# Optimization experiments

Measured on AMD Instinct MI355X. Metric: run time of the kernel, lower is better.

Reference implementation:

```python
import jax, jax.numpy as jnp
import numpy as np

Y_SCALE = 0.01  # fixed weight quantization scale (q_scale of the int8 weights)


def setup_inputs() -> dict:
    key = jax.random.key(0)
    kx, kw, kb = jax.random.split(key, 3)
    B, S, IN, OUT = 4, 2048, 4096, 4096
    x = jax.random.normal(kx, (B, S, IN), dtype=jnp.float32)
    # int8 quantized weights, stored transposed as (in_features, out_features)
    weight_q = jax.random.randint(kw, (IN, OUT), -128, 128, dtype=jnp.int32)
    bias = jax.random.normal(kb, (OUT,), dtype=jnp.float32)
    return {"x": x, "weight_q": weight_q, "bias": bias}


def reference(x, weight_q, bias):
    # Per-batch-sample dynamic activation scale: max(|x_i|)/128 over each [S, IN] slice
    x_scale = jnp.max(jnp.abs(x), axis=(1, 2), keepdims=True) / 128.0  # [B,1,1]
    # int8 quantize: round + clip
    xq = jnp.clip(jnp.round(x / x_scale), -128, 127).astype(jnp.int8)  # [B,S,IN]
    wq = weight_q.astype(jnp.int8)                                      # [IN,OUT]
    c = jax.lax.dot_general(
        xq, wq,
        dimension_numbers=(((2,), (0,)), ((), ())),
        preferred_element_type=jnp.int32,
    )  # [B,S,OUT]
    # dequantize and bias-add
    y = c.astype(jnp.float32) * (x_scale * Y_SCALE)
    return y + bias
```

## Files before the change

kernel.cpp:

```cpp
#include <hip/hip_runtime.h>
#include <stdint.h>

#define K_DIM 4096
#define N_DIM 4096
#define M_DIM 8192
#define S_ROWS 2048
#define NBATCH 4

typedef int v4i __attribute__((ext_vector_type(4)));

__device__ __forceinline__ void gload16(const void* g, void* l) {
    __builtin_amdgcn_global_load_lds(
        (const __attribute__((address_space(1))) unsigned int*)g,
        (__attribute__((address_space(3))) unsigned int*)l, 16, 0, 0);
}

__global__ void absmax_kernel(const float* __restrict__ x, unsigned* __restrict__ amax) {
    int b = blockIdx.y;
    const float4* xb = (const float4*)(x + (size_t)b * S_ROWS * K_DIM);
    int tid = blockIdx.x * 256 + threadIdx.x;
    const int stride = 1024 * 256;
    float m = 0.f;
#pragma unroll
    for (int i = 0; i < 8; ++i) {
        float4 v = xb[tid + i * stride];
        m = fmaxf(m, fmaxf(fmaxf(fabsf(v.x), fabsf(v.y)),
                           fmaxf(fabsf(v.z), fabsf(v.w))));
    }
#pragma unroll
    for (int off = 32; off; off >>= 1)
        m = fmaxf(m, __shfl_xor(m, off));
    __shared__ float red[4];
    if ((threadIdx.x & 63) == 0) red[threadIdx.x >> 6] = m;
    __syncthreads();
    if (threadIdx.x == 0) {
        m = fmaxf(fmaxf(red[0], red[1]), fmaxf(red[2], red[3]));
        atomicMax(&amax[b], __float_as_uint(m));
    }
}

__global__ void quant_kernel(const float* __restrict__ x,
                             const unsigned* __restrict__ amax,
                             char* __restrict__ xq) {
    size_t gid = (size_t)blockIdx.x * 256 + threadIdx.x;
    size_t base = gid * 16;
    int b = (int)(base >> 23);
    float inv = 128.0f / __uint_as_float(amax[b]);
    const float4* xs = (const float4*)(x + base);
    unsigned parts[4];
#pragma unroll
    for (int i = 0; i < 4; ++i) {
        float4 v = xs[i];
        int q0 = max(-128, min(127, (int)rintf(v.x * inv)));
        int q1 = max(-128, min(127, (int)rintf(v.y * inv)));
        int q2 = max(-128, min(127, (int)rintf(v.z * inv)));
        int q3 = max(-128, min(127, (int)rintf(v.w * inv)));
        parts[i] = (q0 & 255) | ((q1 & 255) << 8) | ((q2 & 255) << 16) | ((q3 & 255) << 24);
    }
    *(uint4*)(xq + base) = make_uint4(parts[0], parts[1], parts[2], parts[3]);
}

__global__ void wtrans_kernel(const int* __restrict__ wq, char* __restrict__ wt) {
    __shared__ unsigned lds[64 * 17];
    int t = threadIdx.x;
    int c = t & 63;
    int g = t >> 6;
    int n0 = blockIdx.x * 64;
    int k0 = blockIdx.y * 64;
#pragma unroll
    for (int rep = 0; rep < 4; ++rep) {
        int kb = g * 16 + rep * 4;
        int v0 = wq[(size_t)(k0 + kb + 0) * N_DIM + n0 + c];
        int v1 = wq[(size_t)(k0 + kb + 1) * N_DIM + n0 + c];
        int v2 = wq[(size_t)(k0 + kb + 2) * N_DIM + n0 + c];
        int v3 = wq[(size_t)(k0 + kb + 3) * N_DIM + n0 + c];
        lds[c * 17 + (kb >> 2)] =
            (v0 & 255) | ((v1 & 255) << 8) | ((v2 & 255) << 16) | ((v3 & 255) << 24);
    }
    __syncthreads();
    int row = t >> 2;
    int ch = t & 3;
    uint4 o;
    o.x = lds[row * 17 + ch * 4 + 0];
    o.y = lds[row * 17 + ch * 4 + 1];
    o.z = lds[row * 17 + ch * 4 + 2];
    o.w = lds[row * 17 + ch * 4 + 3];
    *(uint4*)(wt + (size_t)(n0 + row) * K_DIM + k0 + ch * 16) = o;
}

__global__ void gemm_kernel(const char* __restrict__ A,
                            const char* __restrict__ Bt,
                            const float* __restrict__ bias,
                            const unsigned* __restrict__ amax,
                            float* __restrict__ out) {
    __shared__ char As[128 * 64];
    __shared__ char Bs[128 * 64];
    int t = threadIdx.x;
    int l = t & 63;
    int w = t >> 6;
    int wm = w >> 1, wn = w & 1;
    int m0 = blockIdx.y * 128;
    int n0 = blockIdx.x * 128;

    v4i acc[4][4];
#pragma unroll
    for (int i = 0; i < 4; ++i)
#pragma unroll
        for (int j = 0; j < 4; ++j)
            acc[i][j] = (v4i){0, 0, 0, 0};

    int sk = l >> 4;
    int rb = l & 15;

    for (int kt = 0; kt < K_DIM; kt += 64) {
#pragma unroll
        for (int i = 0; i < 2; ++i) {
            int p = (w * 2 + i) * 64 + l;
            int r = p >> 2;
            int s = (p & 3) ^ ((r >> 1) & 3);
            gload16(A + (size_t)(m0 + r) * K_DIM + kt + s * 16, As + p * 16);
            gload16(Bt + (size_t)(n0 + r) * K_DIM + kt + s * 16, Bs + p * 16);
        }
        __syncthreads();

        v4i a[4], bf[4];
#pragma unroll
        for (int mi = 0; mi < 4; ++mi) {
            int row = wm * 64 + mi * 16 + rb;
            a[mi] = *(const v4i*)(As + row * 64 + ((sk ^ ((row >> 1) & 3)) << 4));
        }
#pragma unroll
        for (int ni = 0; ni < 4; ++ni) {
            int row = wn * 64 + ni * 16 + rb;
            bf[ni] = *(const v4i*)(Bs + row * 64 + ((sk ^ ((row >> 1) & 3)) << 4));
        }
#pragma unroll
        for (int mi = 0; mi < 4; ++mi)
#pragma unroll
            for (int ni = 0; ni < 4; ++ni)
                acc[mi][ni] = __builtin_amdgcn_mfma_i32_16x16x64_i8(
                    a[mi], bf[ni], acc[mi][ni], 0, 0, 0);
        __syncthreads();
    }

    float scale = __uint_as_float(amax[m0 >> 11]) * (1.0f / 128.0f) * 0.01f;
    int colb = n0 + wn * 64 + (l & 15);
    int rowb = m0 + wm * 64 + (l >> 4) * 4;
#pragma unroll
    for (int ni = 0; ni < 4; ++ni) {
        float bv = bias[colb + ni * 16];
#pragma unroll
        for (int mi = 0; mi < 4; ++mi) {
#pragma unroll
            for (int rg = 0; rg < 4; ++rg) {
                out[(size_t)(rowb + mi * 16 + rg) * N_DIM + colb + ni * 16] =
                    (float)acc[mi][ni][rg] * scale + bv;
            }
        }
    }
}

extern "C" void kernel_launch(void* const* d_in, const int* in_sizes, int n_in,
                              void* d_out, int out_size, void* d_ws, size_t ws_size,
                              hipStream_t stream) {
    const float* x = (const float*)d_in[0];
    const int* wq = (const int*)d_in[1];
    const float* bias = (const float*)d_in[2];
    float* out = (float*)d_out;

    unsigned* amax = (unsigned*)d_ws;
    char* xq = (char*)d_ws + 256;
    char* wt = (char*)d_ws + 256 + (size_t)M_DIM * K_DIM;

    hipMemsetAsync(d_ws, 0, 16, stream);

    wtrans_kernel<<<dim3(64, 64), 256, 0, stream>>>(wq, wt);
    absmax_kernel<<<dim3(1024, 4), 256, 0, stream>>>(x, amax);
    quant_kernel<<<8192, 256, 0, stream>>>(x, amax, xq);
    gemm_kernel<<<dim3(32, 64), 256, 0, stream>>>(xq, wt, bias, amax, out);
}
```

Baseline: 264.9 us.

## Replace int8 GEMM with 256x256 double-buffered, phase-pipelined 8-wave kernel

```diff
diff --git a/kernel.cpp b/kernel.cpp
--- a/kernel.cpp
+++ b/kernel.cpp
@@ -5,7 +5,7 @@
 #define N_DIM 4096
 #define M_DIM 8192
 #define S_ROWS 2048
-#define NBATCH 4
+#define NT 32
 
 typedef int v4i __attribute__((ext_vector_type(4)));
 
@@ -13,6 +13,12 @@
     __builtin_amdgcn_global_load_lds(
         (const __attribute__((address_space(1))) unsigned int*)g,
         (__attribute__((address_space(3))) unsigned int*)l, 16, 0, 0);
+}
+
+__device__ __forceinline__ void barrier() {
+    asm volatile("" ::: "memory");
+    __builtin_amdgcn_s_barrier();
+    asm volatile("" ::: "memory");
 }
 
 __global__ void absmax_kernel(const float* __restrict__ x, unsigned* __restrict__ amax) {
@@ -88,76 +94,173 @@
     *(uint4*)(wt + (size_t)(n0 + row) * K_DIM + k0 + ch * 16) = o;
 }
 
-__global__ void gemm_kernel(const char* __restrict__ A,
-                            const char* __restrict__ Bt,
-                            const float* __restrict__ bias,
-                            const unsigned* __restrict__ amax,
-                            float* __restrict__ out) {
-    __shared__ char As[128 * 64];
-    __shared__ char Bs[128 * 64];
-    int t = threadIdx.x;
-    int l = t & 63;
-    int w = t >> 6;
-    int wm = w >> 1, wn = w & 1;
-    int m0 = blockIdx.y * 128;
-    int n0 = blockIdx.x * 128;
-
-    v4i acc[4][4];
-#pragma unroll
-    for (int i = 0; i < 4; ++i)
-#pragma unroll
-        for (int j = 0; j < 4; ++j)
-            acc[i][j] = (v4i){0, 0, 0, 0};
-
-    int sk = l >> 4;
-    int rb = l & 15;
-
-    for (int kt = 0; kt < K_DIM; kt += 64) {
-#pragma unroll
-        for (int i = 0; i < 2; ++i) {
-            int p = (w * 2 + i) * 64 + l;
-            int r = p >> 2;
-            int s = (p & 3) ^ ((r >> 1) & 3);
-            gload16(A + (size_t)(m0 + r) * K_DIM + kt + s * 16, As + p * 16);
-            gload16(Bt + (size_t)(n0 + r) * K_DIM + kt + s * 16, Bs + p * 16);
+__global__ __launch_bounds__(512, 2) void gemm8_kernel(
+    const char* __restrict__ A, const char* __restrict__ Bt,
+    const float* __restrict__ bias, const unsigned* __restrict__ amax,
+    float* __restrict__ out) {
+    __shared__ char sm[131072];
+    const int t = threadIdx.x;
+    const int l = t & 63;
+    const int w = t >> 6;
+    const int wm = w >> 2;
+    const int wn = w & 3;
+    const int rb = l & 15;
+    const int sg = l >> 4;
+
+    int bid = blockIdx.x;
+    int swz = (bid & 7) * 64 + (bid >> 3);
+    int mt = swz >> 4, nt = swz & 15;
+    const size_t m0 = (size_t)mt * 256;
+    const size_t n0 = (size_t)nt * 256;
+
+    v4i acc[8][4];
+#pragma unroll
+    for (int i = 0; i < 8; ++i)
+#pragma unroll
+        for (int j = 0; j < 4; ++j) acc[i][j] = (v4i){0, 0, 0, 0};
+
+#define ST_A(tt, h)                                                          \
+    if ((tt) < NT) {                                                         \
+        char* lb = sm + (((tt) & 1) * 65536);                                \
+        const char* gb = A + m0 * K_DIM + (size_t)(tt) * 128;                \
+        _Pragma("unroll")                                                    \
+        for (int j = 0; j < 2; ++j) {                                        \
+            int p = j * 512 + t;                                             \
+            int r7 = p >> 3, sl = p & 7;                                     \
+            int r = (r7 & 63) + ((r7 >> 6) << 7) + ((h) << 6);               \
+            int s = sl ^ (r & 7);                                            \
+            gload16(gb + (size_t)r * K_DIM + s * 16, lb + r * 128 + sl * 16);\
+        }                                                                    \
+    }
+#define ST_B(tt, h)                                                          \
+    if ((tt) < NT) {                                                         \
+        char* lb = sm + (((tt) & 1) * 65536) + 32768;                        \
+        const char* gb = Bt + n0 * K_DIM + (size_t)(tt) * 128;               \
+        _Pragma("unroll")                                                    \
+        for (int j = 0; j < 2; ++j) {                                        \
+            int p = j * 512 + t;                                             \
+            int r7 = p >> 3, sl = p & 7;                                     \
+            int r = ((r7 >> 5) << 6) + ((h) << 5) + (r7 & 31);               \
+            int s = sl ^ (r & 7);                                            \
+            gload16(gb + (size_t)r * K_DIM + s * 16, lb + r * 128 + sl * 16);\
+        }                                                                    \
+    }
+
+    ST_A(0, 0); ST_B(0, 0); ST_A(0, 1); ST_B(0, 1); ST_A(1, 0); ST_B(1, 0);
+
+    v4i aF[4][2], bF[4][2];
+
+    for (int i = 0; i < NT; ++i) {
+        const char* pA = sm + (i & 1) * 65536;
+        const char* pB = pA + 32768;
+        if (i == NT - 1) { asm volatile("s_waitcnt vmcnt(0)" ::: "memory"); }
+        else             { asm volatile("s_waitcnt vmcnt(4)" ::: "memory"); }
+        barrier();
+
+#pragma unroll
+        for (int mi = 0; mi < 4; ++mi)
+#pragma unroll
+            for (int ks = 0; ks < 2; ++ks) {
+                int r = wm * 128 + mi * 16 + rb;
+                aF[mi][ks] = *(const v4i*)(pA + r * 128 + (((ks << 2) + sg) ^ (r & 7)) * 16);
+            }
+#pragma unroll
+        for (int ni = 0; ni < 2; ++ni)
+#pragma unroll
+            for (int ks = 0; ks < 2; ++ks) {
+                int r = wn * 64 + ni * 16 + rb;
+                bF[ni][ks] = *(const v4i*)(pB + r * 128 + (((ks << 2) + sg) ^ (r & 7)) * 16);
+            }
+        ST_A(i + 1, 1);
+        barrier();
+        asm volatile("s_waitcnt lgkmcnt(0)" ::: "memory");
+        __builtin_amdgcn_s_setprio(1);
+#pragma unroll
+        for (int mi = 0; mi < 4; ++mi)
+#pragma unroll
+            for (int ni = 0; ni < 2; ++ni)
+#pragma unroll
+                for (int ks = 0; ks < 2; ++ks)
+                    acc[mi][ni] = __builtin_amdgcn_mfma_i32_16x16x64_i8(
+                        aF[mi][ks], bF[ni][ks], acc[mi][ni], 0, 0, 0);
+        __builtin_amdgcn_s_setprio(0);
+        barrier();
+
+#pragma unroll
+        for (int ni = 2; ni < 4; ++ni)
+#pragma unroll
+            for (int ks = 0; ks < 2; ++ks) {
+                int r = wn * 64 + ni * 16 + rb;
+                bF[ni][ks] = *(const v4i*)(pB + r * 128 + (((ks << 2) + sg) ^ (r & 7)) * 16);
+            }
+        ST_B(i + 1, 1);
+        barrier();
+        asm volatile("s_waitcnt lgkmcnt(0)" ::: "memory");
+        __builtin_amdgcn_s_setprio(1);
+#pragma unroll
+        for (int mi = 0; mi < 4; ++mi)
+#pragma unroll
+            for (int ni = 2; ni < 4; ++ni)
+#pragma unroll
+                for (int ks = 0; ks < 2; ++ks)
+                    acc[mi][ni] = __builtin_amdgcn_mfma_i32_16x16x64_i8(
+                        aF[mi][ks], bF[ni][ks], acc[mi][ni], 0, 0, 0);
+        __builtin_amdgcn_s_setprio(0);
+        barrier();
+
+#pragma unroll
+        for (int mi = 0; mi < 4; ++mi)
+#pragma unroll
+            for (int ks = 0; ks < 2; ++ks) {
+                int r = wm * 128 + 64 + mi * 16 + rb;
+                aF[mi][ks] = *(const v4i*)(pA + r * 128 + (((ks << 2) + sg) ^ (r & 7)) * 16);
+            }
+        ST_A(i + 2, 0);
+        barrier();
+        asm volatile("s_waitcnt lgkmcnt(0)" ::: "memory");
+        __builtin_amdgcn_s_setprio(1);
+#pragma unroll
+        for (int mi = 0; mi < 4; ++mi)
+#pragma unroll
+            for (int ni = 2; ni < 4; ++ni)
+#pragma unroll
+                for (int ks = 0; ks < 2; ++ks)
+                    acc[mi + 4][ni] = __builtin_amdgcn_mfma_i32_16x16x64_i8(
+                        aF[mi][ks], bF[ni][ks], acc[mi + 4][ni], 0, 0, 0);
+        __builtin_amdgcn_s_setprio(0);
+        barrier();
+
+        ST_B(i + 2, 0);
+        barrier();
+        asm volatile("s_waitcnt lgkmcnt(0)" ::: "memory");
+        __builtin_amdgcn_s_setprio(1);
+#pragma unroll
+        for (int mi = 0; mi < 4; ++mi)
+#pragma unroll
+            for (int ni = 0; ni < 2; ++ni)
+#pragma unroll
+                for (int ks = 0; ks < 2; ++ks)
+                    acc[mi + 4][ni] = __builtin_amdgcn_mfma_i32_16x16x64_i8(
+                        aF[mi][ks], bF[ni][ks], acc[mi + 4][ni], 0, 0, 0);
+        __builtin_amdgcn_s_setprio(0);
+        barrier();
+    }
+
+    float scale = __uint_as_float(amax[m0 >> 11]) * (1.0f / 128.0f) * 0.01f;
+#pragma unroll
+    for (int ni = 0; ni < 4; ++ni) {
+        int col = (int)n0 + wn * 64 + ni * 16 + rb;
+        float bv = bias[col];
+#pragma unroll
+        for (int mi = 0; mi < 8; ++mi) {
+            size_t row = m0 + wm * 128 + mi * 16 + sg * 4;
+#pragma unroll
+            for (int rg = 0; rg < 4; ++rg)
+                out[(row + rg) * N_DIM + col] = (float)acc[mi][ni][rg] * scale + bv;
         }
-        __syncthreads();
-
-        v4i a[4], bf[4];
-#pragma unroll
-        for (int mi = 0; mi < 4; ++mi) {
-            int row = wm * 64 + mi * 16 + rb;
-            a[mi] = *(const v4i*)(As + row * 64 + ((sk ^ ((row >> 1) & 3)) << 4));
-        }
-#pragma unroll
-        for (int ni = 0; ni < 4; ++ni) {
-            int row = wn * 64 + ni * 16 + rb;
-            bf[ni] = *(const v4i*)(Bs + row * 64 + ((sk ^ ((row >> 1) & 3)) << 4));
-        }
-#pragma unroll
-        for (int mi = 0; mi < 4; ++mi)
-#pragma unroll
-            for (int ni = 0; ni < 4; ++ni)
-                acc[mi][ni] = __builtin_amdgcn_mfma_i32_16x16x64_i8(
-                    a[mi], bf[ni], acc[mi][ni], 0, 0, 0);
-        __syncthreads();
-    }
-
-    float scale = __uint_as_float(amax[m0 >> 11]) * (1.0f / 128.0f) * 0.01f;
-    int colb = n0 + wn * 64 + (l & 15);
-    int rowb = m0 + wm * 64 + (l >> 4) * 4;
-#pragma unroll
-    for (int ni = 0; ni < 4; ++ni) {
-        float bv = bias[colb + ni * 16];
-#pragma unroll
-        for (int mi = 0; mi < 4; ++mi) {
-#pragma unroll
-            for (int rg = 0; rg < 4; ++rg) {
-                out[(size_t)(rowb + mi * 16 + rg) * N_DIM + colb + ni * 16] =
-                    (float)acc[mi][ni][rg] * scale + bv;
-            }
-        }
-    }
+    }
+#undef ST_A
+#undef ST_B
 }
 
 extern "C" void kernel_launch(void* const* d_in, const int* in_sizes, int n_in,
@@ -177,5 +280,5 @@
     wtrans_kernel<<<dim3(64, 64), 256, 0, stream>>>(wq, wt);
     absmax_kernel<<<dim3(1024, 4), 256, 0, stream>>>(x, amax);
     quant_kernel<<<8192, 256, 0, stream>>>(x, amax, xq);
-    gemm_kernel<<<dim3(32, 64), 256, 0, stream>>>(xq, wt, bias, amax, out);
-}
+    gemm8_kernel<<<dim3(512), 512, 0, stream>>>(xq, wt, bias, amax, out);
+}
```

After: 236.4 us. 10.8% less time.
